# Kernel tuning notes

Hardware: AMD Instinct MI355X
Metric: run time of the kernel (lower is better)

## Reference

```python
import jax, jax.numpy as jnp
import numpy as np

N_NODES = 50000
N_EDGES = 1600000


def setup_inputs() -> dict:
    key = jax.random.key(0)
    ks = jax.random.split(key, 8)
    dims = [1024, 2048, 1024, 512]
    fea = jax.random.normal(ks[0], (N_NODES, dims[0]), dtype=jnp.float32)
    edge_index = jax.random.randint(ks[1], (2, N_EDGES), 0, N_NODES, dtype=jnp.int64)
    edge_vals = jax.random.uniform(ks[2], (N_EDGES,), dtype=jnp.float32)
    # Glorot-ish scaled weights per GCN layer
    W1 = jax.random.normal(ks[3], (dims[0], dims[1]), dtype=jnp.float32) / np.sqrt(dims[0])
    W2 = jax.random.normal(ks[4], (dims[1], dims[2]), dtype=jnp.float32) / np.sqrt(dims[1])
    W3 = jax.random.normal(ks[5], (dims[2], dims[3]), dtype=jnp.float32) / np.sqrt(dims[2])
    b1 = jnp.zeros((dims[1],), dtype=jnp.float32)
    b2 = jnp.zeros((dims[2],), dtype=jnp.float32)
    b3 = jnp.zeros((dims[3],), dtype=jnp.float32)
    return {"fea": fea, "edge_index": edge_index, "edge_vals": edge_vals,
            "W1": W1, "b1": b1, "W2": W2, "b2": b2, "W3": W3, "b3": b3}


def _gcn_layer(x, row, col, edge_vals, W, b):
    # dense transform: [N, din] @ [din, dout] + bias
    support = x @ W + b
    # spmm(adj, support) in COO form: out[row] += val * support[col]
    msgs = support[col] * edge_vals[:, None]          # [E, dout]
    return jax.ops.segment_sum(msgs, row, num_segments=N_NODES)


def reference(fea, edge_index, edge_vals, W1, b1, W2, b2, W3, b3):
    row, col = edge_index[0], edge_index[1]
    h = jax.nn.relu(_gcn_layer(fea, row, col, edge_vals, W1, b1))
    h = jax.nn.relu(_gcn_layer(h, row, col, edge_vals, W2, b2))
    # last layer: no activation
    return _gcn_layer(h, row, col, edge_vals, W3, b3)
```

## Files before the change

kernel.cpp:

```cpp
#include <hip/hip_runtime.h>

typedef unsigned short u16;
using bf16x8 = __attribute__((ext_vector_type(8))) short;
using u16x8  = __attribute__((ext_vector_type(8))) unsigned short;
using f32x4  = __attribute__((ext_vector_type(4))) float;

#define NN 50000
#define NPAD 50048

__device__ __forceinline__ u16 f2b(float f) {
  union { float f; unsigned u; } x; x.f = f;
  unsigned r = x.u + 0x7fffu + ((x.u >> 16) & 1u);
  return (u16)(r >> 16);
}
__device__ __forceinline__ float b2f(u16 h) {
  union { unsigned u; float f; } x; x.u = ((unsigned)h) << 16; return x.f;
}

#define GLOAD_LDS16(g, l) __builtin_amdgcn_global_load_lds( \
    (const __attribute__((address_space(1))) unsigned int*)(g), \
    (__attribute__((address_space(3))) unsigned int*)(l), 16, 0, 0)

__global__ void hist_kernel(const int* __restrict__ rows, const float* __restrict__ vals,
                            int* __restrict__ counts, float* __restrict__ rowsum, int E) {
  int e = blockIdx.x * 256 + threadIdx.x;
  if (e < E) {
    int r = rows[e];
    atomicAdd(&counts[r], 1);
    atomicAdd(&rowsum[r], vals[e]);
  }
}

__global__ void scan_bsum(const int* __restrict__ counts, int* __restrict__ bsum, int n) {
  __shared__ int s[256];
  int t = threadIdx.x;
  int gi = blockIdx.x * 256 + t;
  s[t] = (gi < n) ? counts[gi] : 0;
  __syncthreads();
  for (int d = 128; d > 0; d >>= 1) {
    if (t < d) s[t] += s[t + d];
    __syncthreads();
  }
  if (t == 0) bsum[blockIdx.x] = s[0];
}

__global__ void scan_partials(int* __restrict__ bsum, int nb) {
  __shared__ int s[256];
  int t = threadIdx.x;
  int v = (t < nb) ? bsum[t] : 0;
  s[t] = v;
  __syncthreads();
  for (int d = 1; d < 256; d <<= 1) {
    int x = (t >= d) ? s[t - d] : 0;
    __syncthreads();
    s[t] += x;
    __syncthreads();
  }
  if (t < nb) bsum[t] = s[t] - v;
}

__global__ void scan_final(const int* __restrict__ counts, const int* __restrict__ bsum,
                           int* __restrict__ offs, int n) {
  __shared__ int s[256];
  int t = threadIdx.x;
  int gi = blockIdx.x * 256 + t;
  int v = (gi < n) ? counts[gi] : 0;
  s[t] = v;
  __syncthreads();
  for (int d = 1; d < 256; d <<= 1) {
    int x = (t >= d) ? s[t - d] : 0;
    __syncthreads();
    s[t] += x;
    __syncthreads();
  }
  if (gi <= n) offs[gi] = bsum[blockIdx.x] + s[t] - v;
}

__global__ void scatter_kernel(const int* __restrict__ rows, const int* __restrict__ cols,
                               const float* __restrict__ vals, const int* __restrict__ offs,
                               int* __restrict__ cursor, int* __restrict__ ecol,
                               float* __restrict__ ev2, int E) {
  int e = blockIdx.x * 256 + threadIdx.x;
  if (e < E) {
    int r = rows[e];
    int p = offs[r] + atomicAdd(&cursor[r], 1);
    ecol[p] = cols[e];
    ev2[p] = vals[e];
  }
}

__global__ void conv_f2b4(const float* __restrict__ in, u16* __restrict__ out, int n4) {
  int i = blockIdx.x * 256 + threadIdx.x;
  if (i < n4) {
    float4 f = ((const float4*)in)[i];
    ushort4 o;
    o.x = f2b(f.x); o.y = f2b(f.y); o.z = f2b(f.z); o.w = f2b(f.w);
    ((ushort4*)out)[i] = o;
  }
}

__global__ void transpose_conv(const float* __restrict__ W, u16* __restrict__ Wt, int K, int N) {
  __shared__ float tile[32][33];
  int bx = blockIdx.x * 32;
  int by = blockIdx.y * 32;
  int tx = threadIdx.x;
  int ty = threadIdx.y;
  for (int i = 0; i < 32; i += 8) tile[ty + i][tx] = W[(size_t)(by + ty + i) * N + bx + tx];
  __syncthreads();
  for (int i = 0; i < 32; i += 8) Wt[(size_t)(bx + ty + i) * K + by + tx] = f2b(tile[tx][ty + i]);
}

__global__ __launch_bounds__(256)
void gemm_bt(const u16* __restrict__ A, const u16* __restrict__ Bt,
             const float* __restrict__ bias, const float* __restrict__ rowsum,
             u16* __restrict__ C, int M, int N, int K, int relu) {
  __shared__ u16 As[128 * 32];
  __shared__ u16 Bs[128 * 32];
  const int tid = threadIdx.x;
  const int lane = tid & 63;
  const int wave = tid >> 6;
  const int wm = wave >> 1;
  const int wn = wave & 1;
  const int bm = blockIdx.x * 128;
  const int bn = blockIdx.y * 128;
  const int l15 = lane & 15;
  const int lg = lane >> 4;

  f32x4 acc[4][4];
#pragma unroll
  for (int i = 0; i < 4; i++)
#pragma unroll
    for (int j = 0; j < 4; j++)
#pragma unroll
      for (int k = 0; k < 4; k++) acc[i][j][k] = 0.f;

  const int r = tid >> 2;
  const int c = (tid & 3) << 3;
  const u16* gA = A + (size_t)(bm + r) * K + c;
  const u16* gB = Bt + (size_t)(bn + r) * K + c;
  u16* lA = &As[r * 32 + c];
  u16* lB = &Bs[r * 32 + c];

  for (int k0 = 0; k0 < K; k0 += 32) {
    GLOAD_LDS16(gA, lA);
    GLOAD_LDS16(gA + (size_t)64 * K, lA + 64 * 32);
    GLOAD_LDS16(gB, lB);
    GLOAD_LDS16(gB + (size_t)64 * K, lB + 64 * 32);
    gA += 32;
    gB += 32;
    __syncthreads();
    bf16x8 af[4], bfr[4];
#pragma unroll
    for (int i = 0; i < 4; i++) af[i] = *(const bf16x8*)&As[(wm * 64 + i * 16 + l15) * 32 + lg * 8];
#pragma unroll
    for (int j = 0; j < 4; j++) bfr[j] = *(const bf16x8*)&Bs[(wn * 64 + j * 16 + l15) * 32 + lg * 8];
#pragma unroll
    for (int i = 0; i < 4; i++)
#pragma unroll
      for (int j = 0; j < 4; j++)
        acc[i][j] = __builtin_amdgcn_mfma_f32_16x16x32_bf16(af[i], bfr[j], acc[i][j], 0, 0, 0);
    __syncthreads();
  }

#pragma unroll
  for (int i = 0; i < 4; i++) {
    int row0 = bm + wm * 64 + i * 16 + lg * 4;
#pragma unroll
    for (int rr = 0; rr < 4; rr++) {
      int row = row0 + rr;
      if (row < M) {
        float rs = rowsum ? rowsum[row] : 1.0f;
#pragma unroll
        for (int j = 0; j < 4; j++) {
          int col = bn + wn * 64 + j * 16 + l15;
          float v = acc[i][j][rr] + rs * bias[col];
          if (relu) v = fmaxf(v, 0.f);
          C[(size_t)row * N + col] = f2b(v);
        }
      }
    }
  }
}

template <int DCOLS, int RELU, int OUTF32>
__global__ __launch_bounds__(128)
void spmm2(const int* __restrict__ offs, const int* __restrict__ ecol,
           const float* __restrict__ ev, const u16* __restrict__ X,
           void* __restrict__ outp) {
  constexpr int NT = DCOLS / 8;
  __shared__ int cs[NT];
  __shared__ float vs[NT];
  const int node = blockIdx.x;
  const int t = threadIdx.x;
  const int s0 = offs[node];
  const int e0 = offs[node + 1];
  float acc[8];
#pragma unroll
  for (int k = 0; k < 8; k++) acc[k] = 0.f;
  const u16* __restrict__ Xc = X + (size_t)t * 8;

  for (int base = s0; base < e0; base += NT) {
    const int n = min(NT, e0 - base);
    __syncthreads();
    if (t < n) {
      cs[t] = ecol[base + t];
      vs[t] = ev[base + t];
    }
    __syncthreads();
    int j = 0;
    for (; j + 4 <= n; j += 4) {
      const int c0 = cs[j], c1 = cs[j + 1], c2 = cs[j + 2], c3 = cs[j + 3];
      const float v0 = vs[j], v1 = vs[j + 1], v2 = vs[j + 2], v3 = vs[j + 3];
      u16x8 a0 = *(const u16x8*)(Xc + ((size_t)c0 << 10) * (DCOLS / 1024) + (size_t)c0 * (DCOLS % 1024));
      u16x8 a1 = *(const u16x8*)(Xc + (size_t)c1 * DCOLS);
      u16x8 a2 = *(const u16x8*)(Xc + (size_t)c2 * DCOLS);
      u16x8 a3 = *(const u16x8*)(Xc + (size_t)c3 * DCOLS);
#pragma unroll
      for (int k = 0; k < 8; k++) acc[k] += v0 * b2f(a0[k]);
#pragma unroll
      for (int k = 0; k < 8; k++) acc[k] += v1 * b2f(a1[k]);
#pragma unroll
      for (int k = 0; k < 8; k++) acc[k] += v2 * b2f(a2[k]);
#pragma unroll
      for (int k = 0; k < 8; k++) acc[k] += v3 * b2f(a3[k]);
    }
    for (; j < n; j++) {
      const int c0 = cs[j];
      const float v0 = vs[j];
      u16x8 a0 = *(const u16x8*)(Xc + (size_t)c0 * DCOLS);
#pragma unroll
      for (int k = 0; k < 8; k++) acc[k] += v0 * b2f(a0[k]);
    }
  }

  if (RELU) {
#pragma unroll
    for (int k = 0; k < 8; k++) acc[k] = fmaxf(acc[k], 0.f);
  }
  if (OUTF32) {
    float* o = (float*)outp + (size_t)node * DCOLS + (size_t)t * 8;
    float4 s0v, s1v;
    s0v.x = acc[0]; s0v.y = acc[1]; s0v.z = acc[2]; s0v.w = acc[3];
    s1v.x = acc[4]; s1v.y = acc[5]; s1v.z = acc[6]; s1v.w = acc[7];
    ((float4*)o)[0] = s0v;
    ((float4*)o)[1] = s1v;
  } else {
    u16* o = (u16*)outp + (size_t)node * DCOLS + (size_t)t * 8;
    u16x8 st;
#pragma unroll
    for (int k = 0; k < 8; k++) st[k] = f2b(acc[k]);
    *(u16x8*)o = st;
  }
}

extern "C" void kernel_launch(void* const* d_in, const int* in_sizes, int n_in,
                              void* d_out, int out_size, void* d_ws, size_t ws_size,
                              hipStream_t stream) {
  const float* fea = (const float*)d_in[0];
  const int* ei = (const int*)d_in[1];
  const float* ev = (const float*)d_in[2];
  const float* W1 = (const float*)d_in[3];
  const float* b1 = (const float*)d_in[4];
  const float* W2 = (const float*)d_in[5];
  const float* b2 = (const float*)d_in[6];
  const float* W3 = (const float*)d_in[7];
  const float* b3 = (const float*)d_in[8];
  const int E = in_sizes[1] / 2;
  const int* erow = ei;
  const int* ecol_in = ei + E;

  char* w = (char*)d_ws;
  auto alloc = [&](size_t bytes) {
    char* p = w;
    w += (bytes + 255) & ~(size_t)255;
    return p;
  };
  u16* fea_b = (u16*)alloc((size_t)NPAD * 1024 * 2);
  u16* bufB  = (u16*)alloc((size_t)NPAD * 1024 * 2);
  u16* h1_b  = (u16*)alloc((size_t)NPAD * 2048 * 2);
  u16* t2_b  = (u16*)alloc((size_t)NPAD * 1024 * 2);
  u16* W1t = (u16*)alloc((size_t)2048 * 1024 * 2);
  u16* W2t = (u16*)alloc((size_t)1024 * 2048 * 2);
  u16* W3t = (u16*)alloc((size_t)512 * 1024 * 2);
  float* rowsum = (float*)alloc((size_t)NN * 4);
  int* counts = (int*)alloc((size_t)NN * 4);
  int* cursor = (int*)alloc((size_t)NN * 4);
  int* offs = (int*)alloc((size_t)(NN + 1) * 4);
  int* ecol = (int*)alloc((size_t)E * 4);
  float* ev2 = (float*)alloc((size_t)E * 4);
  int* bsum = (int*)alloc(256 * 4);
  (void)bsum; (void)ws_size; (void)n_in; (void)out_size;

  hipMemsetAsync(rowsum, 0, (size_t)((char*)offs - (char*)rowsum), stream);

  const int eb = (E + 255) / 256;
  const int nb = (NN + 256) / 256;
  hist_kernel<<<eb, 256, 0, stream>>>(erow, ev, counts, rowsum, E);
  scan_bsum<<<nb, 256, 0, stream>>>(counts, bsum, NN);
  scan_partials<<<1, 256, 0, stream>>>(bsum, nb);
  scan_final<<<nb, 256, 0, stream>>>(counts, bsum, offs, NN);
  scatter_kernel<<<eb, 256, 0, stream>>>(erow, ecol_in, ev, offs, cursor, ecol, ev2, E);

  conv_f2b4<<<(NN * 1024 / 4 + 255) / 256, 256, 0, stream>>>(fea, fea_b, NN * 1024 / 4);
  dim3 tb(32, 8);
  transpose_conv<<<dim3(2048 / 32, 1024 / 32), tb, 0, stream>>>(W1, W1t, 1024, 2048);
  transpose_conv<<<dim3(1024 / 32, 2048 / 32), tb, 0, stream>>>(W2, W2t, 2048, 1024);
  transpose_conv<<<dim3(512 / 32, 1024 / 32), tb, 0, stream>>>(W3, W3t, 1024, 512);

  const int MT = (NN + 127) / 128;
  spmm2<1024, 0, 0><<<NN, 128, 0, stream>>>(offs, ecol, ev2, fea_b, bufB);
  gemm_bt<<<dim3(MT, 2048 / 128), 256, 0, stream>>>(bufB, W1t, b1, rowsum, h1_b, NN, 2048, 1024, 1);
  gemm_bt<<<dim3(MT, 1024 / 128), 256, 0, stream>>>(h1_b, W2t, b2, nullptr, t2_b, NN, 1024, 2048, 0);
  spmm2<1024, 1, 0><<<NN, 128, 0, stream>>>(offs, ecol, ev2, t2_b, fea_b);
  gemm_bt<<<dim3(MT, 512 / 128), 256, 0, stream>>>(fea_b, W3t, b3, nullptr, bufB, NN, 512, 1024, 0);
  spmm2<512, 0, 1><<<NN, 64, 0, stream>>>(offs, ecol, ev2, bufB, d_out);
}
```

Measured before the change: 2.248 ms.

## Split SpMM into column-half passes with single-wavefront blocks and direct edge loads

Replaces the SpMM kernel with a 64-thread, one-wavefront variant that reads edge columns and values straight from global memory instead of staging them in LDS behind barriers. Each aggregation now runs as two launches over column halves, so each pass gathers a narrower slice of the feature matrix and is more likely to hit in cache. The last layer uses 4-wide loads over two 256-column halves. The cost is twice the launches, the edge list read twice per layer, and per-thread redundant scalar loads of edge indices.

```diff
diff --git a/kernel.cpp b/kernel.cpp
--- a/kernel.cpp
+++ b/kernel.cpp
@@ -182,74 +182,82 @@
   }
 }
 
-template <int DCOLS, int RELU, int OUTF32>
-__global__ __launch_bounds__(128)
-void spmm2(const int* __restrict__ offs, const int* __restrict__ ecol,
+template <int VEC, int RELU, int OUTF32>
+__global__ __launch_bounds__(64)
+void spmm3(const int* __restrict__ offs, const int* __restrict__ ecol,
            const float* __restrict__ ev, const u16* __restrict__ X,
-           void* __restrict__ outp) {
-  constexpr int NT = DCOLS / 8;
-  __shared__ int cs[NT];
-  __shared__ float vs[NT];
+           void* __restrict__ outp, int stride) {
   const int node = blockIdx.x;
   const int t = threadIdx.x;
   const int s0 = offs[node];
   const int e0 = offs[node + 1];
-  float acc[8];
-#pragma unroll
-  for (int k = 0; k < 8; k++) acc[k] = 0.f;
-  const u16* __restrict__ Xc = X + (size_t)t * 8;
-
-  for (int base = s0; base < e0; base += NT) {
-    const int n = min(NT, e0 - base);
-    __syncthreads();
-    if (t < n) {
-      cs[t] = ecol[base + t];
-      vs[t] = ev[base + t];
-    }
-    __syncthreads();
-    int j = 0;
-    for (; j + 4 <= n; j += 4) {
-      const int c0 = cs[j], c1 = cs[j + 1], c2 = cs[j + 2], c3 = cs[j + 3];
-      const float v0 = vs[j], v1 = vs[j + 1], v2 = vs[j + 2], v3 = vs[j + 3];
-      u16x8 a0 = *(const u16x8*)(Xc + ((size_t)c0 << 10) * (DCOLS / 1024) + (size_t)c0 * (DCOLS % 1024));
-      u16x8 a1 = *(const u16x8*)(Xc + (size_t)c1 * DCOLS);
-      u16x8 a2 = *(const u16x8*)(Xc + (size_t)c2 * DCOLS);
-      u16x8 a3 = *(const u16x8*)(Xc + (size_t)c3 * DCOLS);
-#pragma unroll
-      for (int k = 0; k < 8; k++) acc[k] += v0 * b2f(a0[k]);
-#pragma unroll
-      for (int k = 0; k < 8; k++) acc[k] += v1 * b2f(a1[k]);
-#pragma unroll
-      for (int k = 0; k < 8; k++) acc[k] += v2 * b2f(a2[k]);
-#pragma unroll
-      for (int k = 0; k < 8; k++) acc[k] += v3 * b2f(a3[k]);
-    }
-    for (; j < n; j++) {
-      const int c0 = cs[j];
-      const float v0 = vs[j];
-      u16x8 a0 = *(const u16x8*)(Xc + (size_t)c0 * DCOLS);
-#pragma unroll
-      for (int k = 0; k < 8; k++) acc[k] += v0 * b2f(a0[k]);
-    }
+  float acc[VEC];
+#pragma unroll
+  for (int k = 0; k < VEC; k++) acc[k] = 0.f;
+  const u16* __restrict__ Xc = X + (size_t)t * VEC;
+
+  int j = s0;
+  for (; j + 4 <= e0; j += 4) {
+    const int c0 = ecol[j], c1 = ecol[j + 1], c2 = ecol[j + 2], c3 = ecol[j + 3];
+    const float v0 = ev[j], v1 = ev[j + 1], v2 = ev[j + 2], v3 = ev[j + 3];
+    u16 a0[VEC], a1[VEC], a2[VEC], a3[VEC];
+    if constexpr (VEC == 8) {
+      *(u16x8*)a0 = *(const u16x8*)(Xc + (size_t)c0 * stride);
+      *(u16x8*)a1 = *(const u16x8*)(Xc + (size_t)c1 * stride);
+      *(u16x8*)a2 = *(const u16x8*)(Xc + (size_t)c2 * stride);
+      *(u16x8*)a3 = *(const u16x8*)(Xc + (size_t)c3 * stride);
+    } else {
+      *(ushort4*)a0 = *(const ushort4*)(Xc + (size_t)c0 * stride);
+      *(ushort4*)a1 = *(const ushort4*)(Xc + (size_t)c1 * stride);
+      *(ushort4*)a2 = *(const ushort4*)(Xc + (size_t)c2 * stride);
+      *(ushort4*)a3 = *(const ushort4*)(Xc + (size_t)c3 * stride);
+    }
+#pragma unroll
+    for (int k = 0; k < VEC; k++) acc[k] += v0 * b2f(a0[k]);
+#pragma unroll
+    for (int k = 0; k < VEC; k++) acc[k] += v1 * b2f(a1[k]);
+#pragma unroll
+    for (int k = 0; k < VEC; k++) acc[k] += v2 * b2f(a2[k]);
+#pragma unroll
+    for (int k = 0; k < VEC; k++) acc[k] += v3 * b2f(a3[k]);
+  }
+  for (; j < e0; j++) {
+    const int c0 = ecol[j];
+    const float v0 = ev[j];
+    u16 a0[VEC];
+    if constexpr (VEC == 8) {
+      *(u16x8*)a0 = *(const u16x8*)(Xc + (size_t)c0 * stride);
+    } else {
+      *(ushort4*)a0 = *(const ushort4*)(Xc + (size_t)c0 * stride);
+    }
+#pragma unroll
+    for (int k = 0; k < VEC; k++) acc[k] += v0 * b2f(a0[k]);
   }
 
   if (RELU) {
 #pragma unroll
-    for (int k = 0; k < 8; k++) acc[k] = fmaxf(acc[k], 0.f);
+    for (int k = 0; k < VEC; k++) acc[k] = fmaxf(acc[k], 0.f);
   }
   if (OUTF32) {
-    float* o = (float*)outp + (size_t)node * DCOLS + (size_t)t * 8;
-    float4 s0v, s1v;
-    s0v.x = acc[0]; s0v.y = acc[1]; s0v.z = acc[2]; s0v.w = acc[3];
-    s1v.x = acc[4]; s1v.y = acc[5]; s1v.z = acc[6]; s1v.w = acc[7];
-    ((float4*)o)[0] = s0v;
-    ((float4*)o)[1] = s1v;
+    float* o = (float*)outp + (size_t)node * stride + (size_t)t * VEC;
+#pragma unroll
+    for (int k = 0; k < VEC; k += 4) {
+      float4 st;
+      st.x = acc[k]; st.y = acc[k + 1]; st.z = acc[k + 2]; st.w = acc[k + 3];
+      *(float4*)(o + k) = st;
+    }
   } else {
-    u16* o = (u16*)outp + (size_t)node * DCOLS + (size_t)t * 8;
-    u16x8 st;
-#pragma unroll
-    for (int k = 0; k < 8; k++) st[k] = f2b(acc[k]);
-    *(u16x8*)o = st;
+    u16* o = (u16*)outp + (size_t)node * stride + (size_t)t * VEC;
+    if constexpr (VEC == 8) {
+      u16x8 st;
+#pragma unroll
+      for (int k = 0; k < 8; k++) st[k] = f2b(acc[k]);
+      *(u16x8*)o = st;
+    } else {
+      ushort4 st;
+      st.x = f2b(acc[0]); st.y = f2b(acc[1]); st.z = f2b(acc[2]); st.w = f2b(acc[3]);
+      *(ushort4*)o = st;
+    }
   }
 }
 
@@ -308,10 +316,13 @@
   transpose_conv<<<dim3(512 / 32, 1024 / 32), tb, 0, stream>>>(W3, W3t, 1024, 512);
 
   const int MT = (NN + 127) / 128;
-  spmm2<1024, 0, 0><<<NN, 128, 0, stream>>>(offs, ecol, ev2, fea_b, bufB);
+  spmm3<8, 0, 0><<<NN, 64, 0, stream>>>(offs, ecol, ev2, fea_b, bufB, 1024);
+  spmm3<8, 0, 0><<<NN, 64, 0, stream>>>(offs, ecol, ev2, fea_b + 512, bufB + 512, 1024);
   gemm_bt<<<dim3(MT, 2048 / 128), 256, 0, stream>>>(bufB, W1t, b1, rowsum, h1_b, NN, 2048, 1024, 1);
   gemm_bt<<<dim3(MT, 1024 / 128), 256, 0, stream>>>(h1_b, W2t, b2, nullptr, t2_b, NN, 1024, 2048, 0);
-  spmm2<1024, 1, 0><<<NN, 128, 0, stream>>>(offs, ecol, ev2, t2_b, fea_b);
+  spmm3<8, 1, 0><<<NN, 64, 0, stream>>>(offs, ecol, ev2, t2_b, fea_b, 1024);
+  spmm3<8, 1, 0><<<NN, 64, 0, stream>>>(offs, ecol, ev2, t2_b + 512, fea_b + 512, 1024);
   gemm_bt<<<dim3(MT, 512 / 128), 256, 0, stream>>>(fea_b, W3t, b3, nullptr, bufB, NN, 512, 1024, 0);
-  spmm2<512, 0, 1><<<NN, 64, 0, stream>>>(offs, ecol, ev2, bufB, d_out);
-}
+  spmm3<4, 0, 1><<<NN, 64, 0, stream>>>(offs, ecol, ev2, bufB, d_out, 512);
+  spmm3<4, 0, 1><<<NN, 64, 0, stream>>>(offs, ecol, ev2, bufB + 256, (float*)d_out + 256, 512);
+}
```

New measurement: 2.213 ms. About the same (-1.5%).
